# Optimization experiments

Measured on AMD Instinct MI355X. Metric: run time of the kernel, lower is better.

The kernel has to match this reference:

```python
import jax, jax.numpy as jnp
import numpy as np

N = 100000      # nodes
E = 1600000     # edges
HID = 128       # hidden_dim
HEADS = 4
C = HID // HEADS  # 32 per-head channels
L = 2           # num_layers
G = 64          # graphs in batch


def setup_inputs() -> dict:
    key = jax.random.key(0)
    ks = jax.random.split(key, 24)
    s = 0.1
    inp = {
        'x': jax.random.normal(ks[0], (N, 1), jnp.float32),
        'edge_attr': jax.random.normal(ks[1], (E, 1), jnp.float32),
        'edge_index': jax.random.randint(ks[2], (2, E), 0, N, jnp.int32),
        'batch': jnp.sort(jax.random.randint(ks[3], (N,), 0, G, jnp.int32)),
        # encoders
        'enc_w': jax.random.normal(ks[4], (1, HID), jnp.float32) * s,
        'enc_b': jax.random.normal(ks[5], (HID,), jnp.float32) * s,
        'eenc_w': jax.random.normal(ks[6], (1, HID), jnp.float32) * s,
        'eenc_b': jax.random.normal(ks[7], (HID,), jnp.float32) * s,
        # GATConv params, stacked over layers
        'lin_w': jax.random.normal(ks[8], (L, HID, HID), jnp.float32) * s,
        'att_src': jax.random.normal(ks[9], (L, HEADS, C), jnp.float32) * s,
        'att_dst': jax.random.normal(ks[10], (L, HEADS, C), jnp.float32) * s,
        'att_edge': jax.random.normal(ks[11], (L, HEADS, C), jnp.float32) * s,
        'lin_edge_w': jax.random.normal(ks[12], (L, HID, HID), jnp.float32) * s,
        'conv_b': jax.random.normal(ks[13], (L, HID), jnp.float32) * s,
        # BatchNorm (eval mode, running stats)
        'bn_gamma': jax.random.uniform(ks[14], (L, HID), jnp.float32, 0.5, 1.5),
        'bn_beta': jax.random.normal(ks[15], (L, HID), jnp.float32) * s,
        'bn_mean': jax.random.normal(ks[16], (L, HID), jnp.float32) * s,
        'bn_var': jax.random.uniform(ks[17], (L, HID), jnp.float32, 0.5, 1.5),
        # classifier (num_classes==2 path -> sigmoid, squeeze)
        'w1': jax.random.normal(ks[18], (HID, HID // 2), jnp.float32) * s,
        'b1': jax.random.normal(ks[19], (HID // 2,), jnp.float32) * s,
        'w2': jax.random.normal(ks[20], (HID // 2, 1), jnp.float32) * s,
        'b2': jax.random.normal(ks[21], (1,), jnp.float32) * s,
    }
    return inp


def reference(x, edge_attr, edge_index, batch, enc_w, enc_b, eenc_w, eenc_b,
              lin_w, att_src, att_dst, att_edge, lin_edge_w, conv_b,
              bn_gamma, bn_beta, bn_mean, bn_var, w1, b1, w2, b2):
    src, dst = edge_index[0], edge_index[1]
    h = x @ enc_w + enc_b                      # [N, HID]
    e = edge_attr @ eenc_w + eenc_b            # [E, HID]
    n = h.shape[0]
    nL, H, Ch = att_src.shape[0], att_src.shape[1], att_src.shape[2]
    for l in range(nL):
        identity = h
        xs = (h @ lin_w[l]).reshape(n, H, Ch)            # [N, H, C]
        ee = (e @ lin_edge_w[l]).reshape(-1, H, Ch)      # [E, H, C]
        a_s = jnp.einsum('nhc,hc->nh', xs, att_src[l])
        a_d = jnp.einsum('nhc,hc->nh', xs, att_dst[l])
        a_e = jnp.einsum('ehc,hc->eh', ee, att_edge[l])
        alpha = jax.nn.leaky_relu(a_s[src] + a_d[dst] + a_e, 0.2)  # [E, H]
        # segment softmax over edges grouped by destination node
        amax = jax.ops.segment_max(alpha, dst, num_segments=n)
        amax = jax.lax.stop_gradient(jnp.where(jnp.isfinite(amax), amax, 0.0))
        p = jnp.exp(alpha - amax[dst])
        denom = jax.ops.segment_sum(p, dst, num_segments=n)
        attn = p / (denom[dst] + 1e-16)                  # [E, H]
        msg = (xs[src] * attn[:, :, None]).reshape(-1, H * Ch)
        out = jax.ops.segment_sum(msg, dst, num_segments=n) + conv_b[l]
        # BatchNorm1d (eval mode)
        out = (out - bn_mean[l]) * jax.lax.rsqrt(bn_var[l] + 1e-5) * bn_gamma[l] + bn_beta[l]
        h = jax.nn.relu(out) + identity
    # global mean pool
    cnt = jax.ops.segment_sum(jnp.ones((n,), h.dtype), batch, num_segments=G)
    pooled = jax.ops.segment_sum(h, batch, num_segments=G) / jnp.maximum(cnt, 1.0)[:, None]
    z = jax.nn.relu(pooled @ w1 + b1)
    return jax.nn.sigmoid(z @ w2 + b2)[:, 0]   # [G]
```

## Files before the change

### kernel.cpp

```cpp
#include <hip/hip_runtime.h>
#include <hip/hip_bf16.h>

#define NN 100000
#define EE 1600000
#define HIDD 128
#define GG 64
#define NB 512
#define NPB 196
#define NCH 391
#define CH 4096

typedef short bf16x8 __attribute__((ext_vector_type(8)));
typedef float f32x4 __attribute__((ext_vector_type(4)));

__device__ inline unsigned int f2bf(float f) {
    unsigned int u = __float_as_uint(f);
    return (u + 0x7FFFu + ((u >> 16) & 1u)) >> 16;
}
__device__ inline unsigned int pk2(float a, float b) { return f2bf(a) | (f2bf(b) << 16); }
__device__ inline float blo(unsigned int u) { return __uint_as_float(u << 16); }
__device__ inline float bhi(unsigned int u) { return __uint_as_float(u & 0xFFFF0000u); }


__global__ __launch_bounds__(256) void k_bhist(const int* __restrict__ ei,
                                               int* __restrict__ wg_hist) {
    __shared__ int cnt[NB];
    int t = threadIdx.x;
    cnt[t] = 0; cnt[t + 256] = 0;
    __syncthreads();
    int e0 = blockIdx.x * CH;
    #pragma unroll
    for (int i = 0; i < CH / 256; ++i) {
        int e = e0 + i * 256 + t;
        if (e < EE) {
            unsigned d = (unsigned)ei[EE + e];
            atomicAdd(&cnt[d / NPB], 1);
        }
    }
    __syncthreads();
    wg_hist[blockIdx.x * NB + t] = cnt[t];
    wg_hist[blockIdx.x * NB + 256 + t] = cnt[t + 256];
}

__global__ __launch_bounds__(512) void k_bscan_col(const int* __restrict__ wg_hist,
                                                   int* __restrict__ ofs,
                                                   int* __restrict__ btot) {
    __shared__ int sd[512];
    int b = blockIdx.x;
    int t = threadIdx.x;
    int v = (t < NCH) ? wg_hist[t * NB + b] : 0;
    sd[t] = v;
    __syncthreads();
    for (int off = 1; off < 512; off <<= 1) {
        int u = (t >= off) ? sd[t - off] : 0;
        __syncthreads();
        sd[t] += u;
        __syncthreads();
    }
    if (t < NCH) ofs[t * NB + b] = sd[t] - v;
    if (t == 511) btot[b] = sd[511];
}

__global__ __launch_bounds__(512) void k_bbase(const int* __restrict__ btot,
                                               int* __restrict__ bbase) {
    __shared__ int sd[512];
    int t = threadIdx.x;
    int v = btot[t];
    sd[t] = v;
    __syncthreads();
    for (int off = 1; off < 512; off <<= 1) {
        int u = (t >= off) ? sd[t - off] : 0;
        __syncthreads();
        sd[t] += u;
        __syncthreads();
    }
    bbase[t] = sd[t] - v;
    if (t == 511) bbase[512] = sd[511];
}

__global__ __launch_bounds__(256) void k_bscatter(const int* __restrict__ ei,
                                                  const float* __restrict__ ea,
                                                  const int* __restrict__ ofs,
                                                  const int* __restrict__ bbase,
                                                  uint2* __restrict__ ebuf) {
    __shared__ int lcnt[NB];
    __shared__ int sofs[NB];
    int t = threadIdx.x;
    lcnt[t] = 0; lcnt[t + 256] = 0;
    sofs[t] = ofs[blockIdx.x * NB + t] + bbase[t];
    sofs[t + 256] = ofs[blockIdx.x * NB + 256 + t] + bbase[t + 256];
    __syncthreads();
    int e0 = blockIdx.x * CH;
    #pragma unroll
    for (int i = 0; i < CH / 256; ++i) {
        int e = e0 + i * 256 + t;
        if (e < EE) {
            unsigned s = (unsigned)ei[e];
            unsigned d = (unsigned)ei[EE + e];
            float w = ea[e];
            unsigned b = d / NPB;
            unsigned dloc = d - b * NPB;
            int r = atomicAdd(&lcnt[b], 1);
            ebuf[sofs[b] + r] = make_uint2(s | (dloc << 17), __float_as_uint(w));
        }
    }
}

__global__ __launch_bounds__(256) void k_bsort(const uint2* __restrict__ ebuf,
                                               const int* __restrict__ bbase,
                                               uint2* __restrict__ csr,
                                               int* __restrict__ row_ptr) {
    __shared__ int cnt[NPB];
    __shared__ int sc[256];
    __shared__ int pos[NPB];
    int b = blockIdx.x;
    int t = threadIdx.x;
    int ebeg = bbase[b], eend = bbase[b + 1];
    int n0 = b * NPB;
    int nn = NN - n0; if (nn > NPB) nn = NPB;
    if (t < NPB) cnt[t] = 0;
    __syncthreads();
    for (int j = ebeg + t; j < eend; j += 256) {
        uint2 r = ebuf[j];
        atomicAdd(&cnt[r.x >> 17], 1);
    }
    __syncthreads();
    int v = (t < NPB) ? cnt[t] : 0;
    sc[t] = v;
    __syncthreads();
    for (int off = 1; off < 256; off <<= 1) {
        int u = (t >= off) ? sc[t - off] : 0;
        __syncthreads();
        sc[t] += u;
        __syncthreads();
    }
    int lofs = sc[t] - v;
    if (t < NPB) {
        pos[t] = lofs;
        if (t < nn) row_ptr[n0 + t] = ebeg + lofs;
    }
    __syncthreads();
    for (int j = ebeg + t; j < eend; j += 256) {
        uint2 r = ebuf[j];
        int dloc = r.x >> 17;
        int slot = ebeg + atomicAdd(&pos[dloc], 1);
        csr[slot] = make_uint2(r.x & 0x1FFFFu, r.y);
    }
    if (b == 0 && t == 0) row_ptr[NN] = EE;
}


__global__ void k_derive(const float* __restrict__ enc_w, const float* __restrict__ enc_b,
                         const float* __restrict__ eenc_w, const float* __restrict__ eenc_b,
                         const float* __restrict__ lin_w, const float* __restrict__ lin_edge_w,
                         const float* __restrict__ att_src, const float* __restrict__ att_dst,
                         const float* __restrict__ att_edge,
                         const float* __restrict__ bn_gamma, const float* __restrict__ bn_beta,
                         const float* __restrict__ bn_mean, const float* __restrict__ bn_var,
                         float* __restrict__ cblk, unsigned short* __restrict__ wpk16) {
    int t = threadIdx.x;
    __shared__ float red[128];

    float P = 0.f, Q = 0.f;
    for (int j = 0; j < 128; ++j) {
        float w = lin_w[j * 128 + t];
        P += enc_w[j] * w;
        Q += enc_b[j] * w;
    }
    cblk[t] = P;
    cblk[128 + t] = Q;

    for (int l = 0; l < 2; ++l) {
        float sc = bn_gamma[l * 128 + t] * rsqrtf(bn_var[l * 128 + t] + 1e-5f);
        cblk[256 + l * 128 + t] = sc;
        cblk[512 + l * 128 + t] = bn_beta[l * 128 + t] - bn_mean[l * 128 + t] * sc;
    }

    for (int k = 0; k < 128; ++k) {
        wpk16[t * 128 + k] = (unsigned short)f2bf(lin_w[16384 + k * 128 + t]);
    }

    auto headred = [&](float v, int outbase) {
        red[t] = v;
        __syncthreads();
        if (t < 4) {
            float s = 0.f;
            for (int c = 0; c < 32; ++c) s += red[t * 32 + c];
            cblk[outbase + t] = s;
        }
        __syncthreads();
    };

    headred(P * att_src[t], 768);
    headred(Q * att_src[t], 772);
    headred(P * att_dst[t], 776);
    headred(Q * att_dst[t], 780);

    for (int l = 0; l < 2; ++l) {
        float W1 = 0.f, W2 = 0.f;
        for (int j = 0; j < 128; ++j) {
            float w = lin_edge_w[l * 16384 + j * 128 + t];
            W1 += eenc_w[j] * w;
            W2 += eenc_b[j] * w;
        }
        headred(W1 * att_edge[l * 128 + t], 784 + l * 4);
        headred(W2 * att_edge[l * 128 + t], 792 + l * 4);
    }
}


__global__ __launch_bounds__(256) void k_l0(const uint2* __restrict__ csr,
                                            const int* __restrict__ row_ptr,
                                            const float* __restrict__ x,
                                            const float* __restrict__ cblk,
                                            float* __restrict__ tmp0) {
    int wid = threadIdx.x >> 6, lane = threadIdx.x & 63;
    int n = blockIdx.x * 4 + wid;
    if (n >= NN) return;
    int h = lane & 3, eo = lane >> 2;
    float xdv = x[n];
    float ps = cblk[768 + h], qs = cblk[772 + h];
    float base = xdv * cblk[776 + h] + cblk[780 + h] + cblk[792 + h];
    float au = cblk[784 + h];
    int jb = row_ptr[n], je = row_ptr[n + 1];
    float s = 0.f, sx = 0.f;
    for (int j0 = jb; j0 < je; j0 += 16) {
        int j = j0 + eo;
        if (j < je) {
            uint2 r = csr[j];
            float xsv = x[r.x];
            float w = __uint_as_float(r.y);
            float a = xsv * ps + qs + base + w * au;
            a = (a > 0.f) ? a : 0.2f * a;
            float p = __expf(a);
            s += p;
            sx += p * xsv;
        }
    }
    #pragma unroll
    for (int off = 4; off < 64; off <<= 1) {
        s += __shfl_xor(s, off, 64);
        sx += __shfl_xor(sx, off, 64);
    }
    if (lane < 4) {
        tmp0[(size_t)n * 8 + lane] = s;
        tmp0[(size_t)n * 8 + 4 + lane] = sx;
    }
}

__global__ void k_l0_epi(const float* __restrict__ x, const float* __restrict__ enc_w,
                         const float* __restrict__ enc_b, const float* __restrict__ conv_b,
                         const float* __restrict__ cblk, const float* __restrict__ tmp0,
                         unsigned short* __restrict__ h16) {
    int idx = blockIdx.x * blockDim.x + threadIdx.x;
    if (idx >= NN * HIDD) return;
    int n = idx >> 7, k = idx & 127, h = (k >> 5) & 3;
    float s = tmp0[n * 8 + h];
    float sx = tmp0[n * 8 + 4 + h];
    float inv = 1.f / (s + 1e-16f);
    float agg = (sx * cblk[k] + s * cblk[128 + k]) * inv + conv_b[k];
    float o = agg * cblk[256 + k] + cblk[512 + k];
    float hv = fmaxf(o, 0.f) + x[n] * enc_w[k] + enc_b[k];
    h16[idx] = (unsigned short)f2bf(hv);
}


__global__ __launch_bounds__(256) void k_gemm_mfma(const unsigned short* __restrict__ h16,
                                                   const unsigned short* __restrict__ wpk,
                                                   unsigned short* __restrict__ xs16) {
    int wid = threadIdx.x >> 6, lane = threadIdx.x & 63;
    int rbase = blockIdx.x * 64 + wid * 16;
    int hi = lane >> 4, c15 = lane & 15;

    const bf16x8* hrow = (const bf16x8*)(h16 + (size_t)(rbase + c15) * 128);
    bf16x8 a0 = hrow[hi];
    bf16x8 a1 = hrow[4 + hi];
    bf16x8 a2 = hrow[8 + hi];
    bf16x8 a3 = hrow[12 + hi];

    f32x4 acc[8];
    #pragma unroll
    for (int t8 = 0; t8 < 8; ++t8) {
        const bf16x8* wrow = (const bf16x8*)(wpk + (size_t)(t8 * 16 + c15) * 128);
        f32x4 a_ = {0.f, 0.f, 0.f, 0.f};
        a_ = __builtin_amdgcn_mfma_f32_16x16x32_bf16(a0, wrow[hi], a_, 0, 0, 0);
        a_ = __builtin_amdgcn_mfma_f32_16x16x32_bf16(a1, wrow[4 + hi], a_, 0, 0, 0);
        a_ = __builtin_amdgcn_mfma_f32_16x16x32_bf16(a2, wrow[8 + hi], a_, 0, 0, 0);
        a_ = __builtin_amdgcn_mfma_f32_16x16x32_bf16(a3, wrow[12 + hi], a_, 0, 0, 0);
        acc[t8] = a_;
    }
    #pragma unroll
    for (int j = 0; j < 4; ++j) {
        size_t rb = (size_t)(rbase + hi * 4 + j) * 128;
        #pragma unroll
        for (int t8 = 0; t8 < 8; ++t8) {
            xs16[rb + t8 * 16 + c15] = (unsigned short)f2bf(acc[t8][j]);
        }
    }
}

__global__ void k_asad(const unsigned short* __restrict__ xs16,
                       const float* __restrict__ att_src1, const float* __restrict__ att_dst1,
                       float* __restrict__ a_s, float* __restrict__ a_d) {
    int wid = threadIdx.x >> 6, lane = threadIdx.x & 63;
    int n = blockIdx.x * 4 + wid;
    if (n >= NN) return;
    unsigned int u = *(const unsigned int*)(xs16 + (size_t)n * 128 + lane * 2);
    float v0 = blo(u), v1 = bhi(u);
    float2 as2 = *(const float2*)(att_src1 + lane * 2);
    float2 ad2 = *(const float2*)(att_dst1 + lane * 2);
    float vs = v0 * as2.x + v1 * as2.y;
    float vd = v0 * ad2.x + v1 * ad2.y;
    #pragma unroll
    for (int off = 1; off < 16; off <<= 1) {
        vs += __shfl_xor(vs, off, 64);
        vd += __shfl_xor(vd, off, 64);
    }
    if ((lane & 15) == 0) {
        a_s[n * 4 + (lane >> 4)] = vs;
        a_d[n * 4 + (lane >> 4)] = vd;
    }
}


__global__ __launch_bounds__(256) void k_l1_agg(const unsigned short* __restrict__ xs16,
                                                const uint2* __restrict__ csr,
                                                const float* __restrict__ a_s,
                                                const float* __restrict__ a_d,
                                                const int* __restrict__ row_ptr,
                                                const float* __restrict__ cblk,
                                                const float* __restrict__ conv_b,
                                                unsigned short* __restrict__ outb) {
    int wid = threadIdx.x >> 6, lane = threadIdx.x & 63;
    int n = blockIdx.x * 4 + wid;
    if (n >= NN) return;
    int h = lane >> 4;
    int c0 = lane * 2;

    float adh = a_d[(size_t)n * 4 + h] + cblk[796 + h];
    float au = cblk[788 + h];

    float acc0 = 0.f, acc1 = 0.f, s = 0.f;
    int jb = row_ptr[n], je = row_ptr[n + 1];
    const char* xb = (const char*)xs16;
    int j = jb;
    for (; j + 7 < je; j += 8) {
        uint2 r[8];
        float as[8];
        unsigned int u[8];
        #pragma unroll
        for (int q = 0; q < 8; ++q) r[q] = csr[j + q];
        #pragma unroll
        for (int q = 0; q < 8; ++q) as[q] = a_s[(size_t)r[q].x * 4 + h];
        #pragma unroll
        for (int q = 0; q < 8; ++q)
            u[q] = *(const unsigned int*)(xb + ((size_t)r[q].x << 8) + (lane << 2));
        #pragma unroll
        for (int q = 0; q < 8; ++q) {
            float al = as[q] + adh + __uint_as_float(r[q].y) * au;
            al = (al > 0.f) ? al : 0.2f * al;
            float p = __expf(al);
            s += p;
            acc0 += p * blo(u[q]);
            acc1 += p * bhi(u[q]);
        }
    }
    for (; j + 3 < je; j += 4) {
        uint2 r[4];
        float as[4];
        unsigned int u[4];
        #pragma unroll
        for (int q = 0; q < 4; ++q) r[q] = csr[j + q];
        #pragma unroll
        for (int q = 0; q < 4; ++q) as[q] = a_s[(size_t)r[q].x * 4 + h];
        #pragma unroll
        for (int q = 0; q < 4; ++q)
            u[q] = *(const unsigned int*)(xb + ((size_t)r[q].x << 8) + (lane << 2));
        #pragma unroll
        for (int q = 0; q < 4; ++q) {
            float al = as[q] + adh + __uint_as_float(r[q].y) * au;
            al = (al > 0.f) ? al : 0.2f * al;
            float p = __expf(al);
            s += p;
            acc0 += p * blo(u[q]);
            acc1 += p * bhi(u[q]);
        }
    }
    for (; j < je; ++j) {
        uint2 r0 = csr[j];
        float as0 = a_s[(size_t)r0.x * 4 + h];
        unsigned int u0 = *(const unsigned int*)(xb + ((size_t)r0.x << 8) + (lane << 2));
        float al0 = as0 + adh + __uint_as_float(r0.y) * au;
        al0 = (al0 > 0.f) ? al0 : 0.2f * al0;
        float p0 = __expf(al0);
        s += p0;
        acc0 += p0 * blo(u0);
        acc1 += p0 * bhi(u0);
    }
    float inv = 1.f / (s + 1e-16f);
    float o0 = acc0 * inv + conv_b[128 + c0];
    float o1 = acc1 * inv + conv_b[128 + c0 + 1];
    o0 = o0 * cblk[384 + c0] + cblk[640 + c0];
    o1 = o1 * cblk[384 + c0 + 1] + cblk[640 + c0 + 1];
    unsigned int pk = pk2(fmaxf(o0, 0.f), fmaxf(o1, 0.f));
    *(unsigned int*)(outb + (size_t)n * 128 + c0) = pk;
}


__global__ __launch_bounds__(128) void k_pool(const unsigned short* __restrict__ h16,
                                              const unsigned short* __restrict__ outb,
                                              const int* __restrict__ batch,
                                              float* __restrict__ pooled,
                                              float* __restrict__ gcnt) {
    int t = threadIdx.x;
    int c = (t & 63) * 2;
    int half = t >> 6;
    int n0 = blockIdx.x * 32;
    int gfirst = batch[n0];
    int glast = batch[n0 + 31];
    if (gfirst == glast) {
        float a0 = 0.f, a1 = 0.f;
        #pragma unroll
        for (int i = 0; i < 16; ++i) {
            size_t n = (size_t)(n0 + half + i * 2);
            unsigned int uh = *(const unsigned int*)(h16 + n * 128 + c);
            unsigned int ub = *(const unsigned int*)(outb + n * 128 + c);
            a0 += blo(uh) + blo(ub);
            a1 += bhi(uh) + bhi(ub);
        }
        atomicAdd(&pooled[gfirst * 128 + c], a0);
        atomicAdd(&pooled[gfirst * 128 + c + 1], a1);
        if (t == 0) atomicAdd(&gcnt[gfirst], 32.f);
    } else if (half == 0) {
        float a0 = 0.f, a1 = 0.f;
        int run = 0;
        int gprev = gfirst;
        for (int n = n0; n < n0 + 32; ++n) {
            int g = batch[n];
            if (g != gprev) {
                atomicAdd(&pooled[gprev * 128 + c], a0);
                atomicAdd(&pooled[gprev * 128 + c + 1], a1);
                if (t == 0) atomicAdd(&gcnt[gprev], (float)run);
                a0 = a1 = 0.f;
                run = 0;
                gprev = g;
            }
            unsigned int uh = *(const unsigned int*)(h16 + (size_t)n * 128 + c);
            unsigned int ub = *(const unsigned int*)(outb + (size_t)n * 128 + c);
            a0 += blo(uh) + blo(ub);
            a1 += bhi(uh) + bhi(ub);
            run++;
        }
        atomicAdd(&pooled[gprev * 128 + c], a0);
        atomicAdd(&pooled[gprev * 128 + c + 1], a1);
        if (t == 0) atomicAdd(&gcnt[gprev], (float)run);
    }
}

__global__ void k_head(const float* __restrict__ pooled, const float* __restrict__ gcnt,
                       const float* __restrict__ w1, const float* __restrict__ b1,
                       const float* __restrict__ w2, const float* __restrict__ b2,
                       float* __restrict__ out) {
    int g = blockIdx.x;
    int j = threadIdx.x;
    float inv = 1.f / fmaxf(gcnt[g], 1.f);
    float acc = b1[j];
    for (int k = 0; k < 128; ++k) acc += pooled[g * 128 + k] * inv * w1[k * 64 + j];
    float z = fmaxf(acc, 0.f);
    float v = z * w2[j];
    #pragma unroll
    for (int off = 32; off; off >>= 1) v += __shfl_down(v, off, 64);
    if (j == 0) out[g] = 1.f / (1.f + __expf(-(v + b2[0])));
}


extern "C" void kernel_launch(void* const* d_in, const int* in_sizes, int n_in,
                              void* d_out, int out_size, void* d_ws, size_t ws_size,
                              hipStream_t stream) {
    const float* x        = (const float*)d_in[0];
    const float* ea       = (const float*)d_in[1];
    const int*   ei       = (const int*)d_in[2];
    const int*   batch    = (const int*)d_in[3];
    const float* enc_w    = (const float*)d_in[4];
    const float* enc_b    = (const float*)d_in[5];
    const float* eenc_w   = (const float*)d_in[6];
    const float* eenc_b   = (const float*)d_in[7];
    const float* lin_w    = (const float*)d_in[8];
    const float* att_src  = (const float*)d_in[9];
    const float* att_dst  = (const float*)d_in[10];
    const float* att_edge = (const float*)d_in[11];
    const float* lin_edge = (const float*)d_in[12];
    const float* conv_b   = (const float*)d_in[13];
    const float* bn_gamma = (const float*)d_in[14];
    const float* bn_beta  = (const float*)d_in[15];
    const float* bn_mean  = (const float*)d_in[16];
    const float* bn_var   = (const float*)d_in[17];
    const float* w1       = (const float*)d_in[18];
    const float* b1       = (const float*)d_in[19];
    const float* w2       = (const float*)d_in[20];
    const float* b2       = (const float*)d_in[21];
    float* out = (float*)d_out;

    char* ws = (char*)d_ws;
    size_t off = 0;
    auto alloc = [&](size_t bytes) {
        size_t o = off;
        off = (off + bytes + 511) & ~(size_t)511;
        return o;
    };
    int*    wg_hist = (int*)(ws + alloc((size_t)NCH * NB * 4));
    int*    ofs     = (int*)(ws + alloc((size_t)NCH * NB * 4));
    int*    btot    = (int*)(ws + alloc(NB * 4));
    int*    bbase   = (int*)(ws + alloc((NB + 1) * 4));
    int*    row_ptr = (int*)(ws + alloc((size_t)(NN + 1) * 4));
    uint2*  ebuf    = (uint2*)(ws + alloc((size_t)EE * 8));
    uint2*  csr     = (uint2*)(ws + alloc((size_t)EE * 8));
    float*  cblk    = (float*)(ws + alloc(1024 * 4));
    unsigned short* wpk16 = (unsigned short*)(ws + alloc(128 * 128 * 2));
    float*  tmp0    = (float*)(ws + alloc((size_t)NN * 8 * 4));
    float*  a_s     = (float*)(ws + alloc((size_t)NN * 4 * 4));
    float*  a_d     = (float*)(ws + alloc((size_t)NN * 4 * 4));
    unsigned short* h16  = (unsigned short*)(ws + alloc((size_t)(NN + 64) * HIDD * 2));
    unsigned short* xs16 = (unsigned short*)(ws + alloc((size_t)(NN + 64) * HIDD * 2));
    unsigned short* outb = (unsigned short*)(ws + alloc((size_t)NN * HIDD * 2));
    float*  pooled  = (float*)(ws + alloc(GG * HIDD * 4 + GG * 4));
    float*  gcnt    = pooled + GG * HIDD;

    hipMemsetAsync(pooled, 0, GG * HIDD * 4 + GG * 4, stream);

    const int nwave4 = (NN + 3) / 4;

    k_bhist<<<NCH, 256, 0, stream>>>(ei, wg_hist);
    k_bscan_col<<<NB, 512, 0, stream>>>(wg_hist, ofs, btot);
    k_bbase<<<1, 512, 0, stream>>>(btot, bbase);
    k_bscatter<<<NCH, 256, 0, stream>>>(ei, ea, ofs, bbase, ebuf);
    k_bsort<<<511, 256, 0, stream>>>(ebuf, bbase, csr, row_ptr);

    k_derive<<<1, 128, 0, stream>>>(enc_w, enc_b, eenc_w, eenc_b, lin_w, lin_edge,
                                    att_src, att_dst, att_edge,
                                    bn_gamma, bn_beta, bn_mean, bn_var, cblk, wpk16);

    k_l0<<<nwave4, 256, 0, stream>>>(csr, row_ptr, x, cblk, tmp0);
    k_l0_epi<<<(NN * HIDD + 255) / 256, 256, 0, stream>>>(x, enc_w, enc_b, conv_b, cblk,
                                                          tmp0, h16);

    k_gemm_mfma<<<(NN + 63) / 64, 256, 0, stream>>>(h16, wpk16, xs16);
    k_asad<<<nwave4, 256, 0, stream>>>(xs16, att_src + 128, att_dst + 128, a_s, a_d);
    k_l1_agg<<<nwave4, 256, 0, stream>>>(xs16, csr, a_s, a_d, row_ptr, cblk, conv_b, outb);

    k_pool<<<NN / 32, 128, 0, stream>>>(h16, outb, batch, pooled, gcnt);
    k_head<<<GG, 64, 0, stream>>>(pooled, gcnt, w1, b1, w2, b2, out);
}
```

Measured before the change: 388.7 us.

## Precompute per-edge attention weights in fp16 and stage GEMM output through LDS

Splits layer-1 aggregation into an edge-parallel kernel that computes the exponentiated attention logits per edge (stored as fp16 in the reused ebuf) and an aggregation kernel that only reads src indices, the precomputed weights and the gathered features. This removes the redundant per-lane a_s gather and exp work inside the node loop. It also stages GEMM output through shared memory for coalesced 16-byte stores and moves the weight transpose into a separate LDS-based kernel. The cost is extra src32/dst32 arrays written during sorting, an extra kernel pass over all edges, and fp16 rounding of the attention weights.

```diff
diff --git a/kernel.cpp b/kernel.cpp
--- a/kernel.cpp
+++ b/kernel.cpp
@@ -1,5 +1,6 @@
 #include <hip/hip_runtime.h>
 #include <hip/hip_bf16.h>
+#include <hip/hip_fp16.h>
 
 #define NN 100000
 #define EE 1600000
@@ -109,6 +110,8 @@
 __global__ __launch_bounds__(256) void k_bsort(const uint2* __restrict__ ebuf,
                                                const int* __restrict__ bbase,
                                                uint2* __restrict__ csr,
+                                               int* __restrict__ src32,
+                                               int* __restrict__ dst32,
                                                int* __restrict__ row_ptr) {
     __shared__ int cnt[NPB];
     __shared__ int sc[256];
@@ -144,7 +147,10 @@
         uint2 r = ebuf[j];
         int dloc = r.x >> 17;
         int slot = ebeg + atomicAdd(&pos[dloc], 1);
-        csr[slot] = make_uint2(r.x & 0x1FFFFu, r.y);
+        int s = (int)(r.x & 0x1FFFFu);
+        csr[slot] = make_uint2((unsigned)s, r.y);
+        src32[slot] = s;
+        dst32[slot] = n0 + dloc;
     }
     if (b == 0 && t == 0) row_ptr[NN] = EE;
 }
@@ -157,7 +163,7 @@
                          const float* __restrict__ att_edge,
                          const float* __restrict__ bn_gamma, const float* __restrict__ bn_beta,
                          const float* __restrict__ bn_mean, const float* __restrict__ bn_var,
-                         float* __restrict__ cblk, unsigned short* __restrict__ wpk16) {
+                         float* __restrict__ cblk) {
     int t = threadIdx.x;
     __shared__ float red[128];
 
@@ -174,10 +180,6 @@
         float sc = bn_gamma[l * 128 + t] * rsqrtf(bn_var[l * 128 + t] + 1e-5f);
         cblk[256 + l * 128 + t] = sc;
         cblk[512 + l * 128 + t] = bn_beta[l * 128 + t] - bn_mean[l * 128 + t] * sc;
-    }
-
-    for (int k = 0; k < 128; ++k) {
-        wpk16[t * 128 + k] = (unsigned short)f2bf(lin_w[16384 + k * 128 + t]);
     }
 
     auto headred = [&](float v, int outbase) {
@@ -205,6 +207,21 @@
         }
         headred(W1 * att_edge[l * 128 + t], 784 + l * 4);
         headred(W2 * att_edge[l * 128 + t], 792 + l * 4);
+    }
+}
+
+__global__ __launch_bounds__(256) void k_wpk(const float* __restrict__ lin_w,
+                                             unsigned short* __restrict__ wpk16) {
+    __shared__ float s[128 * 129];
+    int t = threadIdx.x;
+    for (int i = t; i < 16384; i += 256) {
+        int k = i >> 7, c = i & 127;
+        s[k * 129 + c] = lin_w[16384 + i];
+    }
+    __syncthreads();
+    for (int i = t; i < 16384; i += 256) {
+        int c = i >> 7, k = i & 127;
+        wpk16[i] = (unsigned short)f2bf(s[k * 129 + c]);
     }
 }
 
@@ -268,8 +285,10 @@
 __global__ __launch_bounds__(256) void k_gemm_mfma(const unsigned short* __restrict__ h16,
                                                    const unsigned short* __restrict__ wpk,
                                                    unsigned short* __restrict__ xs16) {
+    __shared__ unsigned short st[64 * 136];
     int wid = threadIdx.x >> 6, lane = threadIdx.x & 63;
     int rbase = blockIdx.x * 64 + wid * 16;
+    int rloc = wid * 16;
     int hi = lane >> 4, c15 = lane & 15;
 
     const bf16x8* hrow = (const bf16x8*)(h16 + (size_t)(rbase + c15) * 128);
@@ -291,11 +310,19 @@
     }
     #pragma unroll
     for (int j = 0; j < 4; ++j) {
-        size_t rb = (size_t)(rbase + hi * 4 + j) * 128;
+        int r = rloc + hi * 4 + j;
         #pragma unroll
         for (int t8 = 0; t8 < 8; ++t8) {
-            xs16[rb + t8 * 16 + c15] = (unsigned short)f2bf(acc[t8][j]);
-        }
+            st[r * 136 + t8 * 16 + c15] = (unsigned short)f2bf(acc[t8][j]);
+        }
+    }
+    __syncthreads();
+    uint4* g4 = (uint4*)(xs16 + (size_t)blockIdx.x * 64 * 128);
+    int t = threadIdx.x;
+    #pragma unroll
+    for (int i = t; i < 1024; i += 256) {
+        int r = i >> 4, cw = i & 15;
+        g4[i] = *(const uint4*)(st + r * 136 + cw * 8);
     }
 }
 
@@ -323,10 +350,37 @@
 }
 
 
+__global__ __launch_bounds__(256) void k_l1e(const uint2* __restrict__ csr,
+                                             const int* __restrict__ dst32,
+                                             const float* __restrict__ a_s,
+                                             const float* __restrict__ a_d,
+                                             const float* __restrict__ cblk,
+                                             uint2* __restrict__ p8) {
+    int e = blockIdx.x * blockDim.x + threadIdx.x;
+    if (e >= EE) return;
+    uint2 r = csr[e];
+    int s = (int)r.x;
+    int d = dst32[e];
+    float w = __uint_as_float(r.y);
+    float4 as4 = *(const float4*)(a_s + (size_t)s * 4);
+    float4 ad4 = *(const float4*)(a_d + (size_t)d * 4);
+    float av[4] = {as4.x + ad4.x, as4.y + ad4.y, as4.z + ad4.z, as4.w + ad4.w};
+    unsigned short ph[4];
+    #pragma unroll
+    for (int h = 0; h < 4; ++h) {
+        float a = av[h] + cblk[796 + h] + w * cblk[788 + h];
+        a = (a > 0.f) ? a : 0.2f * a;
+        float p = __expf(a);
+        ph[h] = __half_as_ushort(__float2half(p));
+    }
+    p8[e] = make_uint2((unsigned)ph[0] | ((unsigned)ph[1] << 16),
+                       (unsigned)ph[2] | ((unsigned)ph[3] << 16));
+}
+
+
 __global__ __launch_bounds__(256) void k_l1_agg(const unsigned short* __restrict__ xs16,
-                                                const uint2* __restrict__ csr,
-                                                const float* __restrict__ a_s,
-                                                const float* __restrict__ a_d,
+                                                const int* __restrict__ src32,
+                                                const uint2* __restrict__ p8,
                                                 const int* __restrict__ row_ptr,
                                                 const float* __restrict__ cblk,
                                                 const float* __restrict__ conv_b,
@@ -336,66 +390,42 @@
     if (n >= NN) return;
     int h = lane >> 4;
     int c0 = lane * 2;
-
-    float adh = a_d[(size_t)n * 4 + h] + cblk[796 + h];
-    float au = cblk[788 + h];
+    int hw = (h >> 1) << 2;
+    int hs = (h & 1) * 16;
 
     float acc0 = 0.f, acc1 = 0.f, s = 0.f;
     int jb = row_ptr[n], je = row_ptr[n + 1];
     const char* xb = (const char*)xs16;
+    const char* pb = (const char*)p8;
     int j = jb;
     for (; j + 7 < je; j += 8) {
-        uint2 r[8];
-        float as[8];
+        int sq[8];
+        unsigned int up[8];
         unsigned int u[8];
         #pragma unroll
-        for (int q = 0; q < 8; ++q) r[q] = csr[j + q];
-        #pragma unroll
-        for (int q = 0; q < 8; ++q) as[q] = a_s[(size_t)r[q].x * 4 + h];
+        for (int q = 0; q < 8; ++q) sq[q] = src32[j + q];
         #pragma unroll
         for (int q = 0; q < 8; ++q)
-            u[q] = *(const unsigned int*)(xb + ((size_t)r[q].x << 8) + (lane << 2));
+            up[q] = *(const unsigned int*)(pb + (size_t)(j + q) * 8 + hw);
+        #pragma unroll
+        for (int q = 0; q < 8; ++q)
+            u[q] = *(const unsigned int*)(xb + ((size_t)sq[q] << 8) + (lane << 2));
         #pragma unroll
         for (int q = 0; q < 8; ++q) {
-            float al = as[q] + adh + __uint_as_float(r[q].y) * au;
-            al = (al > 0.f) ? al : 0.2f * al;
-            float p = __expf(al);
+            float p = __half2float(__ushort_as_half((unsigned short)(up[q] >> hs)));
             s += p;
             acc0 += p * blo(u[q]);
             acc1 += p * bhi(u[q]);
         }
     }
-    for (; j + 3 < je; j += 4) {
-        uint2 r[4];
-        float as[4];
-        unsigned int u[4];
-        #pragma unroll
-        for (int q = 0; q < 4; ++q) r[q] = csr[j + q];
-        #pragma unroll
-        for (int q = 0; q < 4; ++q) as[q] = a_s[(size_t)r[q].x * 4 + h];
-        #pragma unroll
-        for (int q = 0; q < 4; ++q)
-            u[q] = *(const unsigned int*)(xb + ((size_t)r[q].x << 8) + (lane << 2));
-        #pragma unroll
-        for (int q = 0; q < 4; ++q) {
-            float al = as[q] + adh + __uint_as_float(r[q].y) * au;
-            al = (al > 0.f) ? al : 0.2f * al;
-            float p = __expf(al);
-            s += p;
-            acc0 += p * blo(u[q]);
-            acc1 += p * bhi(u[q]);
-        }
-    }
     for (; j < je; ++j) {
-        uint2 r0 = csr[j];
-        float as0 = a_s[(size_t)r0.x * 4 + h];
-        unsigned int u0 = *(const unsigned int*)(xb + ((size_t)r0.x << 8) + (lane << 2));
-        float al0 = as0 + adh + __uint_as_float(r0.y) * au;
-        al0 = (al0 > 0.f) ? al0 : 0.2f * al0;
-        float p0 = __expf(al0);
-        s += p0;
-        acc0 += p0 * blo(u0);
-        acc1 += p0 * bhi(u0);
+        int sq = src32[j];
+        unsigned int up = *(const unsigned int*)(pb + (size_t)j * 8 + hw);
+        unsigned int u = *(const unsigned int*)(xb + ((size_t)sq << 8) + (lane << 2));
+        float p = __half2float(__ushort_as_half((unsigned short)(up >> hs)));
+        s += p;
+        acc0 += p * blo(u);
+        acc1 += p * bhi(u);
     }
     float inv = 1.f / (s + 1e-16f);
     float o0 = acc0 * inv + conv_b[128 + c0];
@@ -515,6 +545,8 @@
     int*    row_ptr = (int*)(ws + alloc((size_t)(NN + 1) * 4));
     uint2*  ebuf    = (uint2*)(ws + alloc((size_t)EE * 8));
     uint2*  csr     = (uint2*)(ws + alloc((size_t)EE * 8));
+    int*    src32   = (int*)(ws + alloc((size_t)EE * 4));
+    int*    dst32   = (int*)(ws + alloc((size_t)EE * 4));
     float*  cblk    = (float*)(ws + alloc(1024 * 4));
     unsigned short* wpk16 = (unsigned short*)(ws + alloc(128 * 128 * 2));
     float*  tmp0    = (float*)(ws + alloc((size_t)NN * 8 * 4));
@@ -525,20 +557,23 @@
     unsigned short* outb = (unsigned short*)(ws + alloc((size_t)NN * HIDD * 2));
     float*  pooled  = (float*)(ws + alloc(GG * HIDD * 4 + GG * 4));
     float*  gcnt    = pooled + GG * HIDD;
+    uint2*  p8      = ebuf;
 
     hipMemsetAsync(pooled, 0, GG * HIDD * 4 + GG * 4, stream);
 
     const int nwave4 = (NN + 3) / 4;
+    const int eblk   = (EE + 255) / 256;
 
     k_bhist<<<NCH, 256, 0, stream>>>(ei, wg_hist);
     k_bscan_col<<<NB, 512, 0, stream>>>(wg_hist, ofs, btot);
     k_bbase<<<1, 512, 0, stream>>>(btot, bbase);
     k_bscatter<<<NCH, 256, 0, stream>>>(ei, ea, ofs, bbase, ebuf);
-    k_bsort<<<511, 256, 0, stream>>>(ebuf, bbase, csr, row_ptr);
+    k_bsort<<<511, 256, 0, stream>>>(ebuf, bbase, csr, src32, dst32, row_ptr);
 
     k_derive<<<1, 128, 0, stream>>>(enc_w, enc_b, eenc_w, eenc_b, lin_w, lin_edge,
                                     att_src, att_dst, att_edge,
-                                    bn_gamma, bn_beta, bn_mean, bn_var, cblk, wpk16);
+                                    bn_gamma, bn_beta, bn_mean, bn_var, cblk);
+    k_wpk<<<1, 256, 0, stream>>>(lin_w, wpk16);
 
     k_l0<<<nwave4, 256, 0, stream>>>(csr, row_ptr, x, cblk, tmp0);
     k_l0_epi<<<(NN * HIDD + 255) / 256, 256, 0, stream>>>(x, enc_w, enc_b, conv_b, cblk,
@@ -546,7 +581,8 @@
 
     k_gemm_mfma<<<(NN + 63) / 64, 256, 0, stream>>>(h16, wpk16, xs16);
     k_asad<<<nwave4, 256, 0, stream>>>(xs16, att_src + 128, att_dst + 128, a_s, a_d);
-    k_l1_agg<<<nwave4, 256, 0, stream>>>(xs16, csr, a_s, a_d, row_ptr, cblk, conv_b, outb);
+    k_l1e<<<eblk, 256, 0, stream>>>(csr, dst32, a_s, a_d, cblk, p8);
+    k_l1_agg<<<nwave4, 256, 0, stream>>>(xs16, src32, p8, row_ptr, cblk, conv_b, outb);
 
     k_pool<<<NN / 32, 128, 0, stream>>>(h16, outb, batch, pooled, gcnt);
     k_head<<<GG, 64, 0, stream>>>(pooled, gcnt, w1, b1, w2, b2, out);
```

Result: slower. 435.1 us (+11.9%).

## Fuse attention logits into MFMA GEMM, stage output via LDS, split weight packing

Applied to the files above, without the earlier changes.

Removes the separate k_asad kernel by computing per-head source and destination attention logits from the fp32 GEMM accumulators inside k_gemm_mfma. This uses shuffle reductions and writes float4 per row. The GEMM output is now staged through padded shared memory so it can be written to global memory as coalesced 16-byte stores instead of scattered 2-byte stores. The weight transpose-and-pack moves out of the single-thread-block derive kernel into its own LDS-transposed kernel with coalesced accesses. The logits now come from fp32 values rather than bf16-rounded ones, which slightly changes numerics, and one extra kernel launch is added.

```diff
diff --git a/kernel.cpp b/kernel.cpp
--- a/kernel.cpp
+++ b/kernel.cpp
@@ -157,7 +157,7 @@
                          const float* __restrict__ att_edge,
                          const float* __restrict__ bn_gamma, const float* __restrict__ bn_beta,
                          const float* __restrict__ bn_mean, const float* __restrict__ bn_var,
-                         float* __restrict__ cblk, unsigned short* __restrict__ wpk16) {
+                         float* __restrict__ cblk) {
     int t = threadIdx.x;
     __shared__ float red[128];
 
@@ -174,10 +174,6 @@
         float sc = bn_gamma[l * 128 + t] * rsqrtf(bn_var[l * 128 + t] + 1e-5f);
         cblk[256 + l * 128 + t] = sc;
         cblk[512 + l * 128 + t] = bn_beta[l * 128 + t] - bn_mean[l * 128 + t] * sc;
-    }
-
-    for (int k = 0; k < 128; ++k) {
-        wpk16[t * 128 + k] = (unsigned short)f2bf(lin_w[16384 + k * 128 + t]);
     }
 
     auto headred = [&](float v, int outbase) {
@@ -205,6 +201,21 @@
         }
         headred(W1 * att_edge[l * 128 + t], 784 + l * 4);
         headred(W2 * att_edge[l * 128 + t], 792 + l * 4);
+    }
+}
+
+__global__ __launch_bounds__(256) void k_wpk(const float* __restrict__ lin_w,
+                                             unsigned short* __restrict__ wpk16) {
+    __shared__ float s[128 * 129];
+    int t = threadIdx.x;
+    for (int i = t; i < 16384; i += 256) {
+        int k = i >> 7, c = i & 127;
+        s[k * 129 + c] = lin_w[16384 + i];
+    }
+    __syncthreads();
+    for (int i = t; i < 16384; i += 256) {
+        int c = i >> 7, k = i & 127;
+        wpk16[i] = (unsigned short)f2bf(s[k * 129 + c]);
     }
 }
 
@@ -267,9 +278,15 @@
 
 __global__ __launch_bounds__(256) void k_gemm_mfma(const unsigned short* __restrict__ h16,
                                                    const unsigned short* __restrict__ wpk,
-                                                   unsigned short* __restrict__ xs16) {
+                                                   const float* __restrict__ att_src1,
+                                                   const float* __restrict__ att_dst1,
+                                                   unsigned short* __restrict__ xs16,
+                                                   float* __restrict__ a_s,
+                                                   float* __restrict__ a_d) {
+    __shared__ unsigned short st[64 * 136];
     int wid = threadIdx.x >> 6, lane = threadIdx.x & 63;
     int rbase = blockIdx.x * 64 + wid * 16;
+    int rloc = wid * 16;
     int hi = lane >> 4, c15 = lane & 15;
 
     const bf16x8* hrow = (const bf16x8*)(h16 + (size_t)(rbase + c15) * 128);
@@ -289,36 +306,51 @@
         a_ = __builtin_amdgcn_mfma_f32_16x16x32_bf16(a3, wrow[12 + hi], a_, 0, 0, 0);
         acc[t8] = a_;
     }
+
+    float asw[8], adw[8];
+    #pragma unroll
+    for (int t8 = 0; t8 < 8; ++t8) {
+        asw[t8] = att_src1[t8 * 16 + c15];
+        adw[t8] = att_dst1[t8 * 16 + c15];
+    }
     #pragma unroll
     for (int j = 0; j < 4; ++j) {
-        size_t rb = (size_t)(rbase + hi * 4 + j) * 128;
+        float vs[4], vd[4];
+        #pragma unroll
+        for (int h = 0; h < 4; ++h) {
+            vs[h] = acc[2 * h][j] * asw[2 * h] + acc[2 * h + 1][j] * asw[2 * h + 1];
+            vd[h] = acc[2 * h][j] * adw[2 * h] + acc[2 * h + 1][j] * adw[2 * h + 1];
+        }
+        #pragma unroll
+        for (int off = 1; off < 16; off <<= 1) {
+            #pragma unroll
+            for (int h = 0; h < 4; ++h) {
+                vs[h] += __shfl_xor(vs[h], off, 64);
+                vd[h] += __shfl_xor(vd[h], off, 64);
+            }
+        }
+        if (c15 == 0) {
+            size_t r = (size_t)(rbase + hi * 4 + j) * 4;
+            *(float4*)(a_s + r) = make_float4(vs[0], vs[1], vs[2], vs[3]);
+            *(float4*)(a_d + r) = make_float4(vd[0], vd[1], vd[2], vd[3]);
+        }
+    }
+
+    #pragma unroll
+    for (int j = 0; j < 4; ++j) {
+        int r = rloc + hi * 4 + j;
         #pragma unroll
         for (int t8 = 0; t8 < 8; ++t8) {
-            xs16[rb + t8 * 16 + c15] = (unsigned short)f2bf(acc[t8][j]);
-        }
-    }
-}
-
-__global__ void k_asad(const unsigned short* __restrict__ xs16,
-                       const float* __restrict__ att_src1, const float* __restrict__ att_dst1,
-                       float* __restrict__ a_s, float* __restrict__ a_d) {
-    int wid = threadIdx.x >> 6, lane = threadIdx.x & 63;
-    int n = blockIdx.x * 4 + wid;
-    if (n >= NN) return;
-    unsigned int u = *(const unsigned int*)(xs16 + (size_t)n * 128 + lane * 2);
-    float v0 = blo(u), v1 = bhi(u);
-    float2 as2 = *(const float2*)(att_src1 + lane * 2);
-    float2 ad2 = *(const float2*)(att_dst1 + lane * 2);
-    float vs = v0 * as2.x + v1 * as2.y;
-    float vd = v0 * ad2.x + v1 * ad2.y;
-    #pragma unroll
-    for (int off = 1; off < 16; off <<= 1) {
-        vs += __shfl_xor(vs, off, 64);
-        vd += __shfl_xor(vd, off, 64);
-    }
-    if ((lane & 15) == 0) {
-        a_s[n * 4 + (lane >> 4)] = vs;
-        a_d[n * 4 + (lane >> 4)] = vd;
+            st[r * 136 + t8 * 16 + c15] = (unsigned short)f2bf(acc[t8][j]);
+        }
+    }
+    __syncthreads();
+    uint4* g4 = (uint4*)(xs16 + (size_t)blockIdx.x * 64 * 128);
+    int t = threadIdx.x;
+    #pragma unroll
+    for (int i = t; i < 1024; i += 256) {
+        int r = i >> 4, cw = i & 15;
+        g4[i] = *(const uint4*)(st + r * 136 + cw * 8);
     }
 }
 
@@ -518,8 +550,8 @@
     float*  cblk    = (float*)(ws + alloc(1024 * 4));
     unsigned short* wpk16 = (unsigned short*)(ws + alloc(128 * 128 * 2));
     float*  tmp0    = (float*)(ws + alloc((size_t)NN * 8 * 4));
-    float*  a_s     = (float*)(ws + alloc((size_t)NN * 4 * 4));
-    float*  a_d     = (float*)(ws + alloc((size_t)NN * 4 * 4));
+    float*  a_s     = (float*)(ws + alloc((size_t)(NN + 64) * 4 * 4));
+    float*  a_d     = (float*)(ws + alloc((size_t)(NN + 64) * 4 * 4));
     unsigned short* h16  = (unsigned short*)(ws + alloc((size_t)(NN + 64) * HIDD * 2));
     unsigned short* xs16 = (unsigned short*)(ws + alloc((size_t)(NN + 64) * HIDD * 2));
     unsigned short* outb = (unsigned short*)(ws + alloc((size_t)NN * HIDD * 2));
@@ -538,14 +570,15 @@
 
     k_derive<<<1, 128, 0, stream>>>(enc_w, enc_b, eenc_w, eenc_b, lin_w, lin_edge,
                                     att_src, att_dst, att_edge,
-                                    bn_gamma, bn_beta, bn_mean, bn_var, cblk, wpk16);
+                                    bn_gamma, bn_beta, bn_mean, bn_var, cblk);
+    k_wpk<<<1, 256, 0, stream>>>(lin_w, wpk16);
 
     k_l0<<<nwave4, 256, 0, stream>>>(csr, row_ptr, x, cblk, tmp0);
     k_l0_epi<<<(NN * HIDD + 255) / 256, 256, 0, stream>>>(x, enc_w, enc_b, conv_b, cblk,
                                                           tmp0, h16);
 
-    k_gemm_mfma<<<(NN + 63) / 64, 256, 0, stream>>>(h16, wpk16, xs16);
-    k_asad<<<nwave4, 256, 0, stream>>>(xs16, att_src + 128, att_dst + 128, a_s, a_d);
+    k_gemm_mfma<<<(NN + 63) / 64, 256, 0, stream>>>(h16, wpk16, att_src + 128, att_dst + 128,
+                                                    xs16, a_s, a_d);
     k_l1_agg<<<nwave4, 256, 0, stream>>>(xs16, csr, a_s, a_d, row_ptr, cblk, conv_b, outb);
 
     k_pool<<<NN / 32, 128, 0, stream>>>(h16, outb, batch, pooled, gcnt);
```

Result: no change. 386.4 us (-0.6%).
